# Kernel tuning notes

Hardware: AMD Instinct MI355X
Metric: run time of the kernel (lower is better)

Reference implementation:

```python
import jax, jax.numpy as jnp
import numpy as np

WS = 8            # window_size
SHIFT = WS // 2   # cyclic shift for 'SW' type
HEAD_DIM = 32

def _rel_index(ws):
    # pairwise relative coordinate indices within a window, offset to [0, 2ws-2]
    cord = np.array([[i, j] for i in range(ws) for j in range(ws)])
    rel = cord[:, None, :] - cord[None, :, :] + ws - 1
    return rel[:, :, 0], rel[:, :, 1]

def _shift_mask(h_w, w_w, p):
    # boolean attention mask for shifted windows; True = masked (-inf)
    s = p - SHIFT
    m = np.zeros((h_w, w_w, p, p, p, p), dtype=bool)
    m[-1, :, :s, :, s:, :] = True
    m[-1, :, s:, :, :s, :] = True
    m[:, -1, :, :s, :, s:] = True
    m[:, -1, :, s:, :, :s] = True
    return m.reshape(h_w * w_w, p * p, p * p)

def setup_inputs() -> dict:
    key = jax.random.key(0)
    ks = jax.random.split(key, 6)
    b, H, W, c = 4, 256, 256, 256
    nh = c // HEAD_DIM
    return {
        "x": jax.random.normal(ks[0], (b, H, W, c), jnp.float32),
        "W_qkv": jax.random.normal(ks[1], (c, 3 * c), jnp.float32) * 0.02,
        "b_qkv": jnp.zeros((3 * c,), jnp.float32),
        "rel_pos": jax.random.normal(ks[2], (nh, 2 * WS - 1, 2 * WS - 1), jnp.float32) * 0.02,
        "W_out": jax.random.normal(ks[3], (c, c), jnp.float32) * 0.02,
        "b_out": jnp.zeros((c,), jnp.float32),
    }

def reference(x, W_qkv, b_qkv, rel_pos, W_out, b_out):
    b, H, W, c = x.shape
    nh = c // HEAD_DIM
    scale = HEAD_DIM ** -0.5
    # cyclic shift (type == 'SW')
    x = jnp.roll(x, (-SHIFT, -SHIFT), axis=(1, 2))
    hw, ww = H // WS, W // WS
    nw, p2 = hw * ww, WS * WS
    # partition into windows: [b, nw, p2, c]
    xw = x.reshape(b, hw, WS, ww, WS, c).transpose(0, 1, 3, 2, 4, 5).reshape(b, nw, p2, c)
    # QKV projection; layout of out dim is (3, n_heads, head_dim)
    qkv = (xw @ W_qkv + b_qkv).reshape(b, nw, p2, 3, nh, HEAD_DIM)
    q, k, v = qkv[..., 0, :, :], qkv[..., 1, :, :], qkv[..., 2, :, :]
    # attention scores per head/window: [h, b, nw, p2, p2]
    sim = jnp.einsum('bwphc,bwqhc->hbwpq', q, k) * scale
    ri, rj = _rel_index(WS)
    sim = sim + rel_pos[:, ri, rj][:, None, None]            # relative position bias
    mask = jnp.asarray(_shift_mask(hw, ww, WS))              # [nw, p2, p2]
    sim = jnp.where(mask[None, None], -jnp.inf, sim)
    probs = jax.nn.softmax(sim, axis=-1)
    out = jnp.einsum('hbwpq,bwqhc->bwphc', probs, v).reshape(b, nw, p2, nh * HEAD_DIM)
    out = out @ W_out + b_out
    # un-window: [b, H, W, c_out]
    out = out.reshape(b, hw, ww, WS, WS, -1).transpose(0, 1, 3, 2, 4, 5).reshape(b, H, W, -1)
    return jnp.roll(out, (SHIFT, SHIFT), axis=(1, 2))
```

## Files before the change

kernel.cpp:

```cpp
#include <hip/hip_runtime.h>
#include <hip/hip_bf16.h>

typedef __attribute__((ext_vector_type(4))) float f32x4;
typedef __attribute__((ext_vector_type(2))) unsigned int u32x2;
typedef __attribute__((ext_vector_type(8))) short s16x8;
typedef __attribute__((ext_vector_type(8))) __bf16 bf16v8;
typedef __attribute__((ext_vector_type(8))) _Float16 f16v8;
typedef __attribute__((ext_vector_type(4))) _Float16 f16x4;

#define LDS_XS 0
#define LDS_QS 32768
#define LDS_KS 65536
#define LDS_VT 98304
#define LDS_TOT 131072

__device__ __forceinline__ f32x4 mfma16(s16x8 a, s16x8 b, f32x4 c) {
  return __builtin_amdgcn_mfma_f32_16x16x32_bf16(
      __builtin_bit_cast(bf16v8, a), __builtin_bit_cast(bf16v8, b), c, 0, 0, 0);
}
__device__ __forceinline__ f32x4 mfma16h(s16x8 a, s16x8 b, f32x4 c) {
  return __builtin_amdgcn_mfma_f32_16x16x32_f16(
      __builtin_bit_cast(f16v8, a), __builtin_bit_cast(f16v8, b), c, 0, 0, 0);
}
__device__ __forceinline__ f32x4 mfmah16(f16x4 a, f16x4 b, f32x4 c) {
  return __builtin_amdgcn_mfma_f32_16x16x16f16(a, b, c, 0, 0, 0);
}

__device__ __forceinline__ unsigned int cvt2(float a, float b) {
  __hip_bfloat162 r = __float22bfloat162_rn(make_float2(a, b));
  unsigned int u;
  __builtin_memcpy(&u, &r, 4);
  return u;
}
__device__ __forceinline__ unsigned int cvt2h(float a, float b) {
  auto r = __builtin_amdgcn_cvt_pkrtz(a, b);
  unsigned int u;
  __builtin_memcpy(&u, &r, 4);
  return u;
}
__device__ __forceinline__ f16x4 pack4h(float a, float b, float c, float d) {
  u32x2 u;
  u.x = cvt2h(a, b);
  u.y = cvt2h(c, d);
  f16x4 r;
  __builtin_memcpy(&r, &u, 8);
  return r;
}

__device__ __forceinline__ short f2bf(float f) {
  unsigned u = __float_as_uint(f);
  u += 0x7fffu + ((u >> 16) & 1u);
  return (short)(u >> 16);
}

__device__ __forceinline__ int swz512(int row, int colByte) {
  return row * 512 + (colByte ^ ((row & 7) << 4));
}
__device__ __forceinline__ int swz128(int row, int colByte) {
  return row * 128 + (colByte ^ ((row & 7) << 4));
}

__global__ void prep_w(const float* __restrict__ Wqkv, const float* __restrict__ Wout,
                       const float* __restrict__ relp,
                       short* __restrict__ wqkvT, short* __restrict__ wH,
                       float* __restrict__ relt) {
  int t = blockIdx.x * 256 + threadIdx.x;
  if (t < 768 * 256) {
    int n = t >> 8, k = t & 255;
    wqkvT[t] = f2bf(Wqkv[k * 768 + n]);
  } else if (t < 768 * 256 + 256 * 256) {
    int t2 = t - 768 * 256;
    int n = t2 >> 8, k = t2 & 255;
    _Float16 h = (_Float16)Wout[k * 256 + n];
    unsigned short us;
    __builtin_memcpy(&us, &h, 2);
    wH[t2] = (short)us;
  } else {
    int u = t - 768 * 256 - 256 * 256;
    int r = u & 3, l = (u >> 2) & 63, strip = (u >> 8) & 3;
    int qt = (u >> 10) & 3, h = (u >> 12) & 7, var = (u >> 15) & 3;
    int p = strip * 16 + (l & 15);
    int q = qt * 16 + ((l >> 4) << 2) + r;
    int pi = p >> 3, pj = p & 7, qi = q >> 3, qj = q & 7;
    bool mrow = (var >> 1) & 1, mcol = var & 1;
    bool mk = (mrow && ((pi < 4) != (qi < 4))) || (mcol && ((pj < 4) != (qj < 4)));
    relt[u] = mk ? -1e30f : relp[h * 225 + (pi - qi + 7) * 15 + (pj - qj + 7)];
  }
}

__global__ __launch_bounds__(512, 2) void swin_mfma(
    const float* __restrict__ x, const float* __restrict__ bqkv,
    const float* __restrict__ bout,
    const short* __restrict__ wqkvT, const short* __restrict__ wH,
    const float* __restrict__ relt, float* __restrict__ out)
{
  __shared__ __align__(16) char lds[LDS_TOT];

  const int tx = threadIdx.x;
  const int w  = tx >> 6;
  const int l  = tx & 63;
  const int g  = l >> 4;
  const int li = l & 15;

  const int b   = blockIdx.x >> 10;
  const int wdw = blockIdx.x & 1023;
  const int wh  = wdw >> 5, wwi = wdw & 31;

  for (int i = 0; i < 8; ++i) {
    int idx = tx + i * 512;
    int p = idx >> 6, c4 = idx & 63;
    int pi = p >> 3, pj = p & 7;
    int sr = (wh * 8 + pi + 4) & 255;
    int sc = (wwi * 8 + pj + 4) & 255;
    f32x4 v = *(const f32x4*)(x + ((((size_t)b * 256 + sr) * 256 + sc) * 256 + c4 * 4));
    u32x2 uu;
    uu.x = cvt2(v[0], v[1]);
    uu.y = cvt2(v[2], v[3]);
    *(u32x2*)(lds + LDS_XS + swz512(p, c4 * 8)) = uu;
  }
  __syncthreads();

  {
    f32x4 acc[6][4];
    #pragma unroll
    for (int j = 0; j < 6; ++j)
      #pragma unroll
      for (int rb = 0; rb < 4; ++rb)
        acc[j][rb] = (f32x4){0.f, 0.f, 0.f, 0.f};

    int ocol[6];
    #pragma unroll
    for (int j = 0; j < 4; ++j) ocol[j] = (w * 4 + j) * 16 + li;
    #pragma unroll
    for (int j = 4; j < 6; ++j) ocol[j] = 512 + (w * 2 + (j - 4)) * 16 + li;

    s16x8 bcur[6], bnext[6];
    #pragma unroll
    for (int j = 0; j < 6; ++j)
      bcur[j] = *(const s16x8*)(wqkvT + (size_t)ocol[j] * 256 + g * 8);

    #pragma unroll
    for (int kk = 0; kk < 8; ++kk) {
      s16x8 a[4];
      #pragma unroll
      for (int rb = 0; rb < 4; ++rb)
        a[rb] = *(const s16x8*)(lds + LDS_XS + swz512(rb * 16 + li, kk * 64 + g * 16));
      if (kk < 7) {
        #pragma unroll
        for (int j = 0; j < 6; ++j)
          bnext[j] = *(const s16x8*)(wqkvT + (size_t)ocol[j] * 256 + (kk + 1) * 32 + g * 8);
      }
      #pragma unroll
      for (int j = 0; j < 4; ++j)
        #pragma unroll
        for (int rb = 0; rb < 4; ++rb)
          acc[j][rb] = mfma16(bcur[j], a[rb], acc[j][rb]);
      #pragma unroll
      for (int j = 4; j < 6; ++j)
        #pragma unroll
        for (int rb = 0; rb < 4; ++rb)
          acc[j][rb] = mfma16(a[rb], bcur[j], acc[j][rb]);
      if (kk < 7) {
        #pragma unroll
        for (int j = 0; j < 6; ++j) bcur[j] = bnext[j];
      }
    }

    #pragma unroll
    for (int j = 0; j < 4; ++j) {
      const int cb = w * 4 + j;
      if (cb < 16) {
        f32x4 bq = *(const f32x4*)(bqkv + cb * 16 + g * 4);
        #pragma unroll
        for (int rb = 0; rb < 4; ++rb) {
          const float SC = 0.17677669529663687f;
          u32x2 uu;
          uu.x = cvt2((acc[j][rb][0] + bq[0]) * SC, (acc[j][rb][1] + bq[1]) * SC);
          uu.y = cvt2((acc[j][rb][2] + bq[2]) * SC, (acc[j][rb][3] + bq[3]) * SC);
          *(u32x2*)(lds + LDS_QS + swz512(rb * 16 + li, cb * 32 + g * 8)) = uu;
        }
      } else {
        f32x4 bk = *(const f32x4*)(bqkv + cb * 16 + g * 4);
        #pragma unroll
        for (int rb = 0; rb < 4; ++rb) {
          u32x2 uu;
          uu.x = cvt2(acc[j][rb][0] + bk[0], acc[j][rb][1] + bk[1]);
          uu.y = cvt2(acc[j][rb][2] + bk[2], acc[j][rb][3] + bk[3]);
          *(u32x2*)(lds + LDS_KS + swz512(rb * 16 + li, (cb - 16) * 32 + g * 8)) = uu;
        }
      }
    }
    #pragma unroll
    for (int j = 4; j < 6; ++j) {
      const int d = (w * 2 + (j - 4)) * 16 + li;
      const float bv = bqkv[512 + d];
      #pragma unroll
      for (int rb = 0; rb < 4; ++rb) {
        u32x2 uu;
        uu.x = cvt2h(acc[j][rb][0] + bv, acc[j][rb][1] + bv);
        uu.y = cvt2h(acc[j][rb][2] + bv, acc[j][rb][3] + bv);
        *(u32x2*)(lds + LDS_VT + swz128(d, rb * 32 + g * 8)) = uu;
      }
    }
  }
  __syncthreads();

  {
    const int rvar = ((wh == 31) ? 2 : 0) | ((wwi == 31) ? 1 : 0);
    const int phalf = w & 1, p0 = phalf * 32;

    #pragma unroll 1
    for (int iter = 0; iter < 2; ++iter) {
      const int h = (w >> 1) + iter * 4;

      f32x4 rc[2][4];
      #pragma unroll
      for (int pt = 0; pt < 2; ++pt)
        #pragma unroll
        for (int qt = 0; qt < 4; ++qt)
          rc[pt][qt] = *(const f32x4*)(relt
              + ((((rvar * 8 + h) * 4 + qt) * 4 + (phalf * 2 + pt)) * 64 + l) * 4);

      s16x8 qf[2];
      #pragma unroll
      for (int pt = 0; pt < 2; ++pt)
        qf[pt] = *(const s16x8*)(lds + LDS_QS + swz512(p0 + pt * 16 + li, h * 64 + g * 16));
      s16x8 kf[4];
      #pragma unroll
      for (int qt = 0; qt < 4; ++qt)
        kf[qt] = *(const s16x8*)(lds + LDS_KS + swz512(qt * 16 + li, h * 64 + g * 16));
      f16x4 vf[2][4];
      #pragma unroll
      for (int dt = 0; dt < 2; ++dt)
        #pragma unroll
        for (int qt = 0; qt < 4; ++qt)
          vf[dt][qt] = *(const f16x4*)(lds + LDS_VT
                                       + swz128(h * 32 + dt * 16 + li, qt * 32 + g * 8));

      f32x4 simT[2][4];
      #pragma unroll
      for (int pt = 0; pt < 2; ++pt)
        #pragma unroll
        for (int qt = 0; qt < 4; ++qt)
          simT[pt][qt] = mfma16(kf[qt], qf[pt], rc[pt][qt]);

      float rinv[2];
      f16x4 pa[2][4];
      #pragma unroll
      for (int pt = 0; pt < 2; ++pt) {
        float s = 0.f;
        #pragma unroll
        for (int qt = 0; qt < 4; ++qt) {
          float e0 = __expf(simT[pt][qt][0]);
          float e1 = __expf(simT[pt][qt][1]);
          float e2 = __expf(simT[pt][qt][2]);
          float e3 = __expf(simT[pt][qt][3]);
          s += (e0 + e1) + (e2 + e3);
          pa[pt][qt] = pack4h(e0, e1, e2, e3);
        }
        s += __shfl_xor(s, 16);
        s += __shfl_xor(s, 32);
        rinv[pt] = 1.0f / s;
      }

      f32x4 at[2][2];
      #pragma unroll
      for (int pt = 0; pt < 2; ++pt)
        #pragma unroll
        for (int dt = 0; dt < 2; ++dt)
          at[pt][dt] = (f32x4){0.f, 0.f, 0.f, 0.f};
      #pragma unroll
      for (int qt = 0; qt < 4; ++qt)
        #pragma unroll
        for (int pt = 0; pt < 2; ++pt)
          #pragma unroll
          for (int dt = 0; dt < 2; ++dt)
            at[pt][dt] = mfmah16(vf[dt][qt], pa[pt][qt], at[pt][dt]);

      #pragma unroll
      for (int pt = 0; pt < 2; ++pt)
        #pragma unroll
        for (int dt = 0; dt < 2; ++dt) {
          const f32x4 a4 = at[pt][dt];
          u32x2 hh;
          hh.x = cvt2h(a4[0] * rinv[pt], a4[1] * rinv[pt]);
          hh.y = cvt2h(a4[2] * rinv[pt], a4[3] * rinv[pt]);
          *(u32x2*)(lds + LDS_XS + swz512(p0 + pt * 16 + li, h * 64 + dt * 32 + g * 8)) = hh;
        }
    }
  }
  __syncthreads();

  {
    f32x4 acc2[2][4];
    #pragma unroll
    for (int c = 0; c < 2; ++c)
      #pragma unroll
      for (int rb = 0; rb < 4; ++rb)
        acc2[c][rb] = (f32x4){0.f, 0.f, 0.f, 0.f};

    s16x8 bc[2], bn[2];
    #pragma unroll
    for (int c = 0; c < 2; ++c)
      bc[c] = *(const s16x8*)(wH + (size_t)((w * 2 + c) * 16 + li) * 256 + g * 8);

    #pragma unroll
    for (int kk = 0; kk < 8; ++kk) {
      s16x8 a[4];
      #pragma unroll
      for (int rb = 0; rb < 4; ++rb)
        a[rb] = *(const s16x8*)(lds + LDS_XS + swz512(rb * 16 + li, kk * 64 + g * 16));
      if (kk < 7) {
        #pragma unroll
        for (int c = 0; c < 2; ++c)
          bn[c] = *(const s16x8*)(wH + (size_t)((w * 2 + c) * 16 + li) * 256
                                  + (kk + 1) * 32 + g * 8);
      }
      #pragma unroll
      for (int c = 0; c < 2; ++c)
        #pragma unroll
        for (int rb = 0; rb < 4; ++rb)
          acc2[c][rb] = mfma16h(a[rb], bc[c], acc2[c][rb]);
      if (kk < 7) {
        #pragma unroll
        for (int c = 0; c < 2; ++c) bc[c] = bn[c];
      }
    }

    #pragma unroll
    for (int c = 0; c < 2; ++c) {
      const int n = (w * 2 + c) * 16 + li;
      const float bo = bout[n];
      #pragma unroll
      for (int rb = 0; rb < 4; ++rb)
        #pragma unroll
        for (int r = 0; r < 4; ++r) {
          int m = rb * 16 + g * 4 + r;
          int pi = m >> 3, pj = m & 7;
          int dr = (wh * 8 + pi + 4) & 255;
          int dc = (wwi * 8 + pj + 4) & 255;
          out[(((size_t)b * 256 + dr) * 256 + dc) * 256 + n] = acc2[c][rb][r] + bo;
        }
    }
  }
}

extern "C" void kernel_launch(void* const* d_in, const int* in_sizes, int n_in,
                              void* d_out, int out_size, void* d_ws, size_t ws_size,
                              hipStream_t stream) {
  (void)in_sizes; (void)n_in; (void)out_size; (void)ws_size;
  const float* x    = (const float*)d_in[0];
  const float* Wqkv = (const float*)d_in[1];
  const float* bqkv = (const float*)d_in[2];
  const float* relp = (const float*)d_in[3];
  const float* Wout = (const float*)d_in[4];
  const float* bout = (const float*)d_in[5];
  float* out = (float*)d_out;

  short* wqkvT = (short*)d_ws;
  short* wH    = wqkvT + 768 * 256;
  float* relt  = (float*)(wH + 256 * 256);

  hipLaunchKernelGGL(prep_w, dim3(1536), dim3(256), 0, stream,
                     Wqkv, Wout, relp, wqkvT, wH, relt);
  hipLaunchKernelGGL(swin_mfma, dim3(4096), dim3(512), 0, stream,
                     x, bqkv, bout, wqkvT, wH, relt, out);
}
```

Before: 401.5 us.

## Split QKV/attention/out-proj into two head-halves to shrink LDS and raise occupancy

The fused window kernel now processes heads in two halves. Each half computes Q/K/V for 128 channels, runs attention for 4 heads, and accumulates its partial out-projection. Q/K buffers halve to 256-byte rows, so LDS drops from 128KB to 80KB and launch bounds ask for 4 blocks per CU. The aim is more waves to hide latency. In exchange the kernel gains two extra barriers per half, drops register double-buffering of weight loads, and LDS may still cap residency at 2 blocks.

Measured after the change: 652.0 us. 62.4% more time.

```diff
diff --git a/kernel.cpp b/kernel.cpp
--- a/kernel.cpp
+++ b/kernel.cpp
@@ -8,11 +8,11 @@
 typedef __attribute__((ext_vector_type(8))) _Float16 f16v8;
 typedef __attribute__((ext_vector_type(4))) _Float16 f16x4;
 
-#define LDS_XS 0
-#define LDS_QS 32768
-#define LDS_KS 65536
-#define LDS_VT 98304
-#define LDS_TOT 131072
+#define LDS_X  0
+#define LDS_Q  32768
+#define LDS_K  49152
+#define LDS_VT 65536
+#define LDS_TOT 81920
 
 __device__ __forceinline__ f32x4 mfma16(s16x8 a, s16x8 b, f32x4 c) {
   return __builtin_amdgcn_mfma_f32_16x16x32_bf16(
@@ -55,6 +55,9 @@
 
 __device__ __forceinline__ int swz512(int row, int colByte) {
   return row * 512 + (colByte ^ ((row & 7) << 4));
+}
+__device__ __forceinline__ int swz256(int row, int colByte) {
+  return row * 256 + (colByte ^ ((row & 7) << 4));
 }
 __device__ __forceinline__ int swz128(int row, int colByte) {
   return row * 128 + (colByte ^ ((row & 7) << 4));
@@ -88,7 +91,7 @@
   }
 }
 
-__global__ __launch_bounds__(512, 2) void swin_mfma(
+__global__ __launch_bounds__(512, 4) void swin_mfma(
     const float* __restrict__ x, const float* __restrict__ bqkv,
     const float* __restrict__ bout,
     const short* __restrict__ wqkvT, const short* __restrict__ wH,
@@ -105,6 +108,7 @@
   const int b   = blockIdx.x >> 10;
   const int wdw = blockIdx.x & 1023;
   const int wh  = wdw >> 5, wwi = wdw & 31;
+  const int rvar = ((wh == 31) ? 2 : 0) | ((wwi == 31) ? 1 : 0);
 
   for (int i = 0; i < 8; ++i) {
     int idx = tx + i * 512;
@@ -116,133 +120,100 @@
     u32x2 uu;
     uu.x = cvt2(v[0], v[1]);
     uu.y = cvt2(v[2], v[3]);
-    *(u32x2*)(lds + LDS_XS + swz512(p, c4 * 8)) = uu;
+    *(u32x2*)(lds + LDS_X + swz512(p, c4 * 8)) = uu;
   }
   __syncthreads();
 
-  {
-    f32x4 acc[6][4];
+  f32x4 acc2[2][4];
+  #pragma unroll
+  for (int c = 0; c < 2; ++c)
     #pragma unroll
-    for (int j = 0; j < 6; ++j)
-      #pragma unroll
-      for (int rb = 0; rb < 4; ++rb)
-        acc[j][rb] = (f32x4){0.f, 0.f, 0.f, 0.f};
-
-    int ocol[6];
-    #pragma unroll
-    for (int j = 0; j < 4; ++j) ocol[j] = (w * 4 + j) * 16 + li;
-    #pragma unroll
-    for (int j = 4; j < 6; ++j) ocol[j] = 512 + (w * 2 + (j - 4)) * 16 + li;
-
-    s16x8 bcur[6], bnext[6];
-    #pragma unroll
-    for (int j = 0; j < 6; ++j)
-      bcur[j] = *(const s16x8*)(wqkvT + (size_t)ocol[j] * 256 + g * 8);
-
-    #pragma unroll
-    for (int kk = 0; kk < 8; ++kk) {
-      s16x8 a[4];
-      #pragma unroll
-      for (int rb = 0; rb < 4; ++rb)
-        a[rb] = *(const s16x8*)(lds + LDS_XS + swz512(rb * 16 + li, kk * 64 + g * 16));
-      if (kk < 7) {
-        #pragma unroll
-        for (int j = 0; j < 6; ++j)
-          bnext[j] = *(const s16x8*)(wqkvT + (size_t)ocol[j] * 256 + (kk + 1) * 32 + g * 8);
-      }
-      #pragma unroll
-      for (int j = 0; j < 4; ++j)
+    for (int rb = 0; rb < 4; ++rb)
+      acc2[c][rb] = (f32x4){0.f, 0.f, 0.f, 0.f};
+
+  #pragma unroll 1
+  for (int hf = 0; hf < 2; ++hf) {
+    {
+      f32x4 accq[4], acck[4], accv[4];
+      #pragma unroll
+      for (int rb = 0; rb < 4; ++rb) {
+        accq[rb] = (f32x4){0.f, 0.f, 0.f, 0.f};
+        acck[rb] = (f32x4){0.f, 0.f, 0.f, 0.f};
+        accv[rb] = (f32x4){0.f, 0.f, 0.f, 0.f};
+      }
+      const size_t oq = (size_t)(hf * 128 + w * 16 + li) * 256;
+      const size_t ok = (size_t)(256 + hf * 128 + w * 16 + li) * 256;
+      const size_t ov = (size_t)(512 + hf * 128 + w * 16 + li) * 256;
+
+      #pragma unroll
+      for (int kk = 0; kk < 8; ++kk) {
+        s16x8 a[4];
         #pragma unroll
         for (int rb = 0; rb < 4; ++rb)
-          acc[j][rb] = mfma16(bcur[j], a[rb], acc[j][rb]);
-      #pragma unroll
-      for (int j = 4; j < 6; ++j)
-        #pragma unroll
-        for (int rb = 0; rb < 4; ++rb)
-          acc[j][rb] = mfma16(a[rb], bcur[j], acc[j][rb]);
-      if (kk < 7) {
-        #pragma unroll
-        for (int j = 0; j < 6; ++j) bcur[j] = bnext[j];
-      }
-    }
-
-    #pragma unroll
-    for (int j = 0; j < 4; ++j) {
-      const int cb = w * 4 + j;
-      if (cb < 16) {
-        f32x4 bq = *(const f32x4*)(bqkv + cb * 16 + g * 4);
+          a[rb] = *(const s16x8*)(lds + LDS_X + swz512(rb * 16 + li, kk * 64 + g * 16));
+        s16x8 bq = *(const s16x8*)(wqkvT + oq + kk * 32 + g * 8);
+        s16x8 bk = *(const s16x8*)(wqkvT + ok + kk * 32 + g * 8);
+        s16x8 bv = *(const s16x8*)(wqkvT + ov + kk * 32 + g * 8);
         #pragma unroll
         for (int rb = 0; rb < 4; ++rb) {
-          const float SC = 0.17677669529663687f;
-          u32x2 uu;
-          uu.x = cvt2((acc[j][rb][0] + bq[0]) * SC, (acc[j][rb][1] + bq[1]) * SC);
-          uu.y = cvt2((acc[j][rb][2] + bq[2]) * SC, (acc[j][rb][3] + bq[3]) * SC);
-          *(u32x2*)(lds + LDS_QS + swz512(rb * 16 + li, cb * 32 + g * 8)) = uu;
-        }
-      } else {
-        f32x4 bk = *(const f32x4*)(bqkv + cb * 16 + g * 4);
+          accq[rb] = mfma16(bq, a[rb], accq[rb]);
+          acck[rb] = mfma16(bk, a[rb], acck[rb]);
+          accv[rb] = mfma16(a[rb], bv, accv[rb]);
+        }
+      }
+
+      {
+        f32x4 bq4 = *(const f32x4*)(bqkv + hf * 128 + w * 16 + g * 4);
+        const float SC = 0.17677669529663687f;
         #pragma unroll
         for (int rb = 0; rb < 4; ++rb) {
           u32x2 uu;
-          uu.x = cvt2(acc[j][rb][0] + bk[0], acc[j][rb][1] + bk[1]);
-          uu.y = cvt2(acc[j][rb][2] + bk[2], acc[j][rb][3] + bk[3]);
-          *(u32x2*)(lds + LDS_KS + swz512(rb * 16 + li, (cb - 16) * 32 + g * 8)) = uu;
+          uu.x = cvt2((accq[rb][0] + bq4[0]) * SC, (accq[rb][1] + bq4[1]) * SC);
+          uu.y = cvt2((accq[rb][2] + bq4[2]) * SC, (accq[rb][3] + bq4[3]) * SC);
+          *(u32x2*)(lds + LDS_Q + swz256(rb * 16 + li, w * 32 + g * 8)) = uu;
+        }
+      }
+      {
+        f32x4 bk4 = *(const f32x4*)(bqkv + 256 + hf * 128 + w * 16 + g * 4);
+        #pragma unroll
+        for (int rb = 0; rb < 4; ++rb) {
+          u32x2 uu;
+          uu.x = cvt2(acck[rb][0] + bk4[0], acck[rb][1] + bk4[1]);
+          uu.y = cvt2(acck[rb][2] + bk4[2], acck[rb][3] + bk4[3]);
+          *(u32x2*)(lds + LDS_K + swz256(rb * 16 + li, w * 32 + g * 8)) = uu;
+        }
+      }
+      {
+        const int d = w * 16 + li;
+        const float bv = bqkv[512 + hf * 128 + d];
+        #pragma unroll
+        for (int rb = 0; rb < 4; ++rb) {
+          u32x2 uu;
+          uu.x = cvt2h(accv[rb][0] + bv, accv[rb][1] + bv);
+          uu.y = cvt2h(accv[rb][2] + bv, accv[rb][3] + bv);
+          *(u32x2*)(lds + LDS_VT + swz128(d, rb * 32 + g * 8)) = uu;
         }
       }
     }
-    #pragma unroll
-    for (int j = 4; j < 6; ++j) {
-      const int d = (w * 2 + (j - 4)) * 16 + li;
-      const float bv = bqkv[512 + d];
-      #pragma unroll
-      for (int rb = 0; rb < 4; ++rb) {
-        u32x2 uu;
-        uu.x = cvt2h(acc[j][rb][0] + bv, acc[j][rb][1] + bv);
-        uu.y = cvt2h(acc[j][rb][2] + bv, acc[j][rb][3] + bv);
-        *(u32x2*)(lds + LDS_VT + swz128(d, rb * 32 + g * 8)) = uu;
-      }
-    }
-  }
-  __syncthreads();
-
-  {
-    const int rvar = ((wh == 31) ? 2 : 0) | ((wwi == 31) ? 1 : 0);
-    const int phalf = w & 1, p0 = phalf * 32;
-
-    #pragma unroll 1
-    for (int iter = 0; iter < 2; ++iter) {
-      const int h = (w >> 1) + iter * 4;
-
-      f32x4 rc[2][4];
-      #pragma unroll
-      for (int pt = 0; pt < 2; ++pt)
-        #pragma unroll
-        for (int qt = 0; qt < 4; ++qt)
-          rc[pt][qt] = *(const f32x4*)(relt
-              + ((((rvar * 8 + h) * 4 + qt) * 4 + (phalf * 2 + pt)) * 64 + l) * 4);
-
-      s16x8 qf[2];
-      #pragma unroll
-      for (int pt = 0; pt < 2; ++pt)
-        qf[pt] = *(const s16x8*)(lds + LDS_QS + swz512(p0 + pt * 16 + li, h * 64 + g * 16));
-      s16x8 kf[4];
-      #pragma unroll
-      for (int qt = 0; qt < 4; ++qt)
-        kf[qt] = *(const s16x8*)(lds + LDS_KS + swz512(qt * 16 + li, h * 64 + g * 16));
-      f16x4 vf[2][4];
-      #pragma unroll
-      for (int dt = 0; dt < 2; ++dt)
-        #pragma unroll
-        for (int qt = 0; qt < 4; ++qt)
-          vf[dt][qt] = *(const f16x4*)(lds + LDS_VT
-                                       + swz128(h * 32 + dt * 16 + li, qt * 32 + g * 8));
+    __syncthreads();
+
+    {
+      const int h = w >> 1;
+      const int ah = hf * 4 + h;
+      const int phalf = w & 1, p0 = phalf * 32;
 
       f32x4 simT[2][4];
       #pragma unroll
-      for (int pt = 0; pt < 2; ++pt)
-        #pragma unroll
-        for (int qt = 0; qt < 4; ++qt)
-          simT[pt][qt] = mfma16(kf[qt], qf[pt], rc[pt][qt]);
+      for (int pt = 0; pt < 2; ++pt) {
+        s16x8 qf = *(const s16x8*)(lds + LDS_Q + swz256(p0 + pt * 16 + li, h * 64 + g * 16));
+        #pragma unroll
+        for (int qt = 0; qt < 4; ++qt) {
+          f32x4 rc = *(const f32x4*)(relt
+              + ((((rvar * 8 + ah) * 4 + qt) * 4 + (phalf * 2 + pt)) * 64 + l) * 4);
+          s16x8 kf = *(const s16x8*)(lds + LDS_K + swz256(qt * 16 + li, h * 64 + g * 16));
+          simT[pt][qt] = mfma16(kf, qf, rc);
+        }
+      }
 
       float rinv[2];
       f16x4 pa[2][4];
@@ -270,12 +241,15 @@
         for (int dt = 0; dt < 2; ++dt)
           at[pt][dt] = (f32x4){0.f, 0.f, 0.f, 0.f};
       #pragma unroll
-      for (int qt = 0; qt < 4; ++qt)
-        #pragma unroll
-        for (int pt = 0; pt < 2; ++pt)
-          #pragma unroll
-          for (int dt = 0; dt < 2; ++dt)
-            at[pt][dt] = mfmah16(vf[dt][qt], pa[pt][qt], at[pt][dt]);
+      for (int qt = 0; qt < 4; ++qt) {
+        f16x4 vf0 = *(const f16x4*)(lds + LDS_VT + swz128(h * 32 + li, qt * 32 + g * 8));
+        f16x4 vf1 = *(const f16x4*)(lds + LDS_VT + swz128(h * 32 + 16 + li, qt * 32 + g * 8));
+        #pragma unroll
+        for (int pt = 0; pt < 2; ++pt) {
+          at[pt][0] = mfmah16(vf0, pa[pt][qt], at[pt][0]);
+          at[pt][1] = mfmah16(vf1, pa[pt][qt], at[pt][1]);
+        }
+      }
 
       #pragma unroll
       for (int pt = 0; pt < 2; ++pt)
@@ -285,63 +259,45 @@
           u32x2 hh;
           hh.x = cvt2h(a4[0] * rinv[pt], a4[1] * rinv[pt]);
           hh.y = cvt2h(a4[2] * rinv[pt], a4[3] * rinv[pt]);
-          *(u32x2*)(lds + LDS_XS + swz512(p0 + pt * 16 + li, h * 64 + dt * 32 + g * 8)) = hh;
+          *(u32x2*)(lds + LDS_Q + swz256(p0 + pt * 16 + li, h * 64 + dt * 32 + g * 8)) = hh;
         }
     }
+    __syncthreads();
+
+    {
+      #pragma unroll
+      for (int kk = 0; kk < 4; ++kk) {
+        s16x8 a[4];
+        #pragma unroll
+        for (int rb = 0; rb < 4; ++rb)
+          a[rb] = *(const s16x8*)(lds + LDS_Q + swz256(rb * 16 + li, kk * 64 + g * 16));
+        #pragma unroll
+        for (int c = 0; c < 2; ++c) {
+          s16x8 bc = *(const s16x8*)(wH + (size_t)((w * 2 + c) * 16 + li) * 256
+                                     + hf * 128 + kk * 32 + g * 8);
+          #pragma unroll
+          for (int rb = 0; rb < 4; ++rb)
+            acc2[c][rb] = mfma16h(a[rb], bc, acc2[c][rb]);
+        }
+      }
+    }
+    if (hf == 0) __syncthreads();
   }
-  __syncthreads();
-
-  {
-    f32x4 acc2[2][4];
+
+  #pragma unroll
+  for (int c = 0; c < 2; ++c) {
+    const int n = (w * 2 + c) * 16 + li;
+    const float bo = bout[n];
     #pragma unroll
-    for (int c = 0; c < 2; ++c)
-      #pragma unroll
-      for (int rb = 0; rb < 4; ++rb)
-        acc2[c][rb] = (f32x4){0.f, 0.f, 0.f, 0.f};
-
-    s16x8 bc[2], bn[2];
-    #pragma unroll
-    for (int c = 0; c < 2; ++c)
-      bc[c] = *(const s16x8*)(wH + (size_t)((w * 2 + c) * 16 + li) * 256 + g * 8);
-
-    #pragma unroll
-    for (int kk = 0; kk < 8; ++kk) {
-      s16x8 a[4];
-      #pragma unroll
-      for (int rb = 0; rb < 4; ++rb)
-        a[rb] = *(const s16x8*)(lds + LDS_XS + swz512(rb * 16 + li, kk * 64 + g * 16));
-      if (kk < 7) {
-        #pragma unroll
-        for (int c = 0; c < 2; ++c)
-          bn[c] = *(const s16x8*)(wH + (size_t)((w * 2 + c) * 16 + li) * 256
-                                  + (kk + 1) * 32 + g * 8);
-      }
-      #pragma unroll
-      for (int c = 0; c < 2; ++c)
-        #pragma unroll
-        for (int rb = 0; rb < 4; ++rb)
-          acc2[c][rb] = mfma16h(a[rb], bc[c], acc2[c][rb]);
-      if (kk < 7) {
-        #pragma unroll
-        for (int c = 0; c < 2; ++c) bc[c] = bn[c];
-      }
-    }
-
-    #pragma unroll
-    for (int c = 0; c < 2; ++c) {
-      const int n = (w * 2 + c) * 16 + li;
-      const float bo = bout[n];
-      #pragma unroll
-      for (int rb = 0; rb < 4; ++rb)
-        #pragma unroll
-        for (int r = 0; r < 4; ++r) {
-          int m = rb * 16 + g * 4 + r;
-          int pi = m >> 3, pj = m & 7;
-          int dr = (wh * 8 + pi + 4) & 255;
-          int dc = (wwi * 8 + pj + 4) & 255;
-          out[(((size_t)b * 256 + dr) * 256 + dc) * 256 + n] = acc2[c][rb][r] + bo;
-        }
-    }
+    for (int rb = 0; rb < 4; ++rb)
+      #pragma unroll
+      for (int r = 0; r < 4; ++r) {
+        int m = rb * 16 + g * 4 + r;
+        int pi = m >> 3, pj = m & 7;
+        int dr = (wh * 8 + pi + 4) & 255;
+        int dc = (wwi * 8 + pj + 4) & 255;
+        out[(((size_t)b * 256 + dr) * 256 + dc) * 256 + n] = acc2[c][rb][r] + bo;
+      }
   }
 }
 
```
